# Performance work log

Hardware: AMD Instinct MI355X
Metric: run time of the kernel (lower is better)

## Reference

```python
import jax, jax.numpy as jnp
import numpy as np

N, D_IN, D_OUT, N_CTRS, K = 16384, 64, 64, 512, 16


def setup_inputs() -> dict:
    key = jax.random.key(0)
    k1, k2, k3, k4 = jax.random.split(key, 4)
    x = jax.random.normal(k1, (N, D_IN), dtype=jnp.float32)
    ctrs = jax.random.normal(k2, (N_CTRS, D_IN), dtype=jnp.float32)
    Wv = jax.random.normal(k3, (N_CTRS, D_IN, D_OUT), dtype=jnp.float32) * 0.02
    Ov = jax.random.normal(k4, (N_CTRS, D_OUT), dtype=jnp.float32) * 0.02
    return {"x": x, "ctrs": ctrs, "Wv": Wv, "Ov": Ov, "k": K}


def reference(x, ctrs, Wv, Ov, k):
    n = x.shape[0]
    # squared distances via expansion (same math as sum((x-c)^2), avoids [n,C,d] blowup)
    x2 = jnp.sum(x * x, axis=1, keepdims=True)            # [n,1]
    c2 = jnp.sum(ctrs * ctrs, axis=1)                     # [C]
    dist_sq = x2 + c2[None, :] - 2.0 * (x @ ctrs.T)       # [n,C]
    # k nearest centers; softmax over negative squared distances of the k selected
    neg_top, idx = jax.lax.top_k(-dist_sq, k)             # [n,k] each
    scores = jax.nn.softmax(neg_top, axis=1)              # [n,k]
    # dense soft-assignment matrix (only k nonzeros per row), as in the torch code
    A = jnp.zeros_like(dist_sq).at[jnp.arange(n)[:, None], idx].set(scores)  # [n,C]
    # per-token affine mix: sum_c A[n,c] * (x[n] @ Wv[c] + Ov[c])
    scored_weights = jnp.einsum('nc,cgp->ngp', A, Wv)     # [n,d_in,d_out]
    out = jnp.einsum('ngp,ng->np', scored_weights, x) + A @ Ov  # [n,d_out]
    return out
```

## Files before the change

### kernel.cpp

```cpp
#include <hip/hip_runtime.h>
#include <hip/hip_fp16.h>

#define N_TOK 16384
#define D 64
#define NC 512
#define KSEL 16
#define NPAIR (N_TOK * KSEL)
#define PADCAP 327168

typedef __attribute__((ext_vector_type(8))) short short8;
typedef __attribute__((ext_vector_type(8))) unsigned short ushort8;
typedef __attribute__((ext_vector_type(16))) float float16;

__device__ __forceinline__ unsigned fkey(float f) {
    unsigned u = __float_as_uint(f);
    return (u & 0x80000000u) ? ~u : (u | 0x80000000u);
}
__device__ __forceinline__ float funkey(unsigned k) {
    unsigned u = (k & 0x80000000u) ? (k & 0x7fffffffu) : ~k;
    return __uint_as_float(u);
}
__device__ __forceinline__ unsigned short bfr(float f) {
    unsigned u = __float_as_uint(f);
    return (unsigned short)((u + 0x7FFFu + ((u >> 16) & 1u)) >> 16);
}
__device__ __forceinline__ float b2f(unsigned short h) {
    return __uint_as_float((unsigned)h << 16);
}
__device__ __forceinline__ unsigned pk2(unsigned short a, unsigned short b) {
    return (unsigned)a | ((unsigned)b << 16);
}

__device__ __forceinline__ void ins16(unsigned (&run)[16], unsigned k) {
    #pragma unroll
    for (int r = 0; r < 16; ++r) {
        unsigned mx = run[r] > k ? run[r] : k;
        unsigned mn = run[r] > k ? k : run[r];
        run[r] = mx; k = mn;
    }
}

__global__ __launch_bounds__(256, 4) void topk14_kernel(
    const float* __restrict__ x, const float* __restrict__ ctrs,
    unsigned* __restrict__ pk) {
    __shared__ __align__(16) unsigned char pool[35328];
    unsigned short* Cbf = (unsigned short*)pool;
    unsigned* Sbk = (unsigned*)pool;
    unsigned* mbp = (unsigned*)pool;
    float* c2s = (float*)(pool + 34816);

    const int t = threadIdx.x;
    const int lane = t & 63;
    const int wv = t >> 6;
    const int mrow = lane & 31;
    const int half = lane >> 5;
    const int tb = blockIdx.x >> 2;
    const int p = blockIdx.x & 3;
    const int base = tb * 64;
    const int cbase = p * 128;
    const int trow = (wv & 1) * 32;
    const int cgrp = (wv >> 1) * 64;

    {
        const int r = t >> 1, q = t & 1;
        const float4* cp = (const float4*)(ctrs + (cbase + r) * D + q * 32);
        unsigned short* Ch = Cbf + r * 136 + q * 32;
        float s2 = 0.f;
        #pragma unroll
        for (int i = 0; i < 8; ++i) {
            float4 v = cp[i];
            s2 += v.x * v.x + v.y * v.y + v.z * v.z + v.w * v.w;
            unsigned short h0 = bfr(v.x), h1 = bfr(v.y), h2 = bfr(v.z), h3 = bfr(v.w);
            unsigned short l0 = bfr(v.x - b2f(h0)), l1 = bfr(v.y - b2f(h1));
            unsigned short l2 = bfr(v.z - b2f(h2)), l3 = bfr(v.w - b2f(h3));
            *(uint2*)(Ch + 4 * i)      = make_uint2(pk2(h0, h1), pk2(h2, h3));
            *(uint2*)(Ch + 64 + 4 * i) = make_uint2(pk2(l0, l1), pk2(l2, l3));
        }
        s2 += __shfl_xor(s2, 1);
        c2s[r] = s2;
    }

    short8 ah[4], al[4];
    {
        const float* xp = x + (base + trow + mrow) * D + half * 8;
        #pragma unroll
        for (int kt = 0; kt < 4; ++kt) {
            float4 u = *(const float4*)(xp + kt * 16);
            float4 v = *(const float4*)(xp + kt * 16 + 4);
            float c[8] = {u.x, u.y, u.z, u.w, v.x, v.y, v.z, v.w};
            #pragma unroll
            for (int j = 0; j < 8; ++j) {
                unsigned short h = bfr(c[j]);
                ah[kt][j] = (short)h;
                al[kt][j] = (short)bfr(c[j] - b2f(h));
            }
        }
    }
    __syncthreads();

    float16 acc0 = {0.f,0.f,0.f,0.f,0.f,0.f,0.f,0.f,0.f,0.f,0.f,0.f,0.f,0.f,0.f,0.f};
    float16 acc1 = acc0;

    const unsigned short* B0 = Cbf + (cgrp + mrow) * 136 + half * 8;
    const unsigned short* B1 = Cbf + (cgrp + 32 + mrow) * 136 + half * 8;
    #pragma unroll
    for (int kt = 0; kt < 4; ++kt) {
        short8 bh0 = *(const short8*)(B0 + kt * 16);
        short8 bh1 = *(const short8*)(B1 + kt * 16);
        short8 bl0 = *(const short8*)(B0 + 64 + kt * 16);
        short8 bl1 = *(const short8*)(B1 + 64 + kt * 16);
        acc0 = __builtin_amdgcn_mfma_f32_32x32x16_bf16(ah[kt], bh0, acc0, 0, 0, 0);
        acc1 = __builtin_amdgcn_mfma_f32_32x32x16_bf16(ah[kt], bh1, acc1, 0, 0, 0);
        acc0 = __builtin_amdgcn_mfma_f32_32x32x16_bf16(al[kt], bh0, acc0, 0, 0, 0);
        acc1 = __builtin_amdgcn_mfma_f32_32x32x16_bf16(al[kt], bh1, acc1, 0, 0, 0);
        acc0 = __builtin_amdgcn_mfma_f32_32x32x16_bf16(ah[kt], bl0, acc0, 0, 0, 0);
        acc1 = __builtin_amdgcn_mfma_f32_32x32x16_bf16(ah[kt], bl1, acc1, 0, 0, 0);
    }
    __syncthreads();

    {
        float ca = c2s[cgrp + mrow];
        float cb = c2s[cgrp + 32 + mrow];
        #pragma unroll
        for (int reg = 0; reg < 16; ++reg) {
            int tokrow = trow + (reg & 3) + 8 * (reg >> 2) + 4 * half;
            float sa = fmaf(2.f, acc0[reg], -ca);
            float sb = fmaf(2.f, acc1[reg], -cb);
            Sbk[tokrow * 132 + cgrp + mrow] =
                (fkey(sa) & 0xFFFFFE00u) | (unsigned)(cbase + cgrp + mrow);
            Sbk[tokrow * 132 + cgrp + 32 + mrow] =
                (fkey(sb) & 0xFFFFFE00u) | (unsigned)(cbase + cgrp + 32 + mrow);
        }
    }
    __syncthreads();

    const int tok = t & 63;
    const int h = t >> 6;
    unsigned run[16];
    #pragma unroll
    for (int r = 0; r < 16; ++r) run[r] = 0u;
    #pragma unroll
    for (int i = 0; i < 8; ++i) {
        int cq = ((i + tok) & 7) ^ ((tok >> 3) & 7);
        uint4 kv = *(const uint4*)(Sbk + tok * 132 + 32 * h + 4 * cq);
        ins16(run, kv.x); ins16(run, kv.y); ins16(run, kv.z); ins16(run, kv.w);
    }
    __syncthreads();

    {
        uint4* dst = (uint4*)(mbp + tok * 68 + h * 16);
        dst[0] = make_uint4(run[0], run[1], run[2], run[3]);
        dst[1] = make_uint4(run[4], run[5], run[6], run[7]);
        dst[2] = make_uint4(run[8], run[9], run[10], run[11]);
        dst[3] = make_uint4(run[12], run[13], run[14], run[15]);
    }
    __syncthreads();

    if (t < 64) {
        const unsigned* pm = mbp + t * 68;
        unsigned hv[4]; int pos[4];
        #pragma unroll
        for (int w = 0; w < 4; ++w) { pos[w] = 0; hv[w] = pm[w * 16]; }
        unsigned mm[16];
        #pragma unroll
        for (int r = 0; r < 16; ++r) {
            unsigned m = hv[0];
            #pragma unroll
            for (int w = 1; w < 4; ++w) m = m > hv[w] ? m : hv[w];
            mm[r] = m;
            #pragma unroll
            for (int w = 0; w < 4; ++w) {
                if (hv[w] == m) {
                    ++pos[w];
                    hv[w] = (pos[w] < 16) ? pm[w * 16 + pos[w]] : 0u;
                }
            }
        }
        uint4* dst = (uint4*)(pk + (size_t)(base + t) * 64 + p * 16);
        dst[0] = make_uint4(mm[0], mm[1], mm[2], mm[3]);
        dst[1] = make_uint4(mm[4], mm[5], mm[6], mm[7]);
        dst[2] = make_uint4(mm[8], mm[9], mm[10], mm[11]);
        dst[3] = make_uint4(mm[12], mm[13], mm[14], mm[15]);
    }
}

__global__ __launch_bounds__(256) void topmerge_kernel(
    const unsigned* __restrict__ pk, float* __restrict__ scores,
    int* __restrict__ sidx, int* __restrict__ hist) {
    __shared__ int lhist[NC];
    const int t = threadIdx.x;
    lhist[t] = 0; lhist[t + 256] = 0;
    __syncthreads();
    const int n = blockIdx.x * 256 + t;
    const unsigned* p = pk + (size_t)n * 64;
    unsigned h[4]; int pos[4];
    #pragma unroll
    for (int w = 0; w < 4; ++w) { pos[w] = 0; h[w] = p[w * 16]; }
    float vals[16]; int ids[16];
    #pragma unroll
    for (int r = 0; r < KSEL; ++r) {
        unsigned m = h[0];
        #pragma unroll
        for (int w = 1; w < 4; ++w) m = m > h[w] ? m : h[w];
        vals[r] = funkey(m);
        ids[r] = (int)(m & 511u);
        #pragma unroll
        for (int w = 0; w < 4; ++w) {
            if (h[w] == m) {
                ++pos[w];
                h[w] = (pos[w] < KSEL) ? p[w * 16 + pos[w]] : 0u;
            }
        }
    }
    float mx = vals[0];
    float e[16]; float sum = 0.f;
    #pragma unroll
    for (int r = 0; r < KSEL; ++r) { e[r] = __expf(vals[r] - mx); sum += e[r]; }
    float inv = 1.f / sum;
    #pragma unroll
    for (int q = 0; q < 4; ++q) {
        *(float4*)(scores + n * KSEL + 4 * q) =
            make_float4(e[4*q] * inv, e[4*q+1] * inv, e[4*q+2] * inv, e[4*q+3] * inv);
        *(int4*)(sidx + n * KSEL + 4 * q) =
            make_int4(ids[4*q], ids[4*q+1], ids[4*q+2], ids[4*q+3]);
    }
    #pragma unroll
    for (int r = 0; r < KSEL; ++r) atomicAdd(&lhist[ids[r]], 1);
    __syncthreads();
    { int hv = lhist[t]; if (hv) atomicAdd(&hist[t], hv); }
    { int hv = lhist[t + 256]; if (hv) atomicAdd(&hist[t + 256], hv); }
}

__global__ __launch_bounds__(512) void scan2_kernel(const int* __restrict__ hist,
                                                    int* __restrict__ cursor,
                                                    int* __restrict__ meta) {
    __shared__ int buf[2][NC];
    int t = threadIdx.x;
    int pad = (hist[t] + 127) & ~127;
    buf[0][t] = pad;
    __syncthreads();
    int a = 0;
    for (int d = 1; d < NC; d <<= 1) {
        int val = buf[a][t] + (t >= d ? buf[a][t - d] : 0);
        buf[1 - a][t] = val;
        __syncthreads();
        a = 1 - a;
    }
    int incl = buf[a][t];
    cursor[t] = incl - pad;
    if (t == NC - 1) meta[0] = incl;
}

__global__ __launch_bounds__(256) void scatter4_kernel(
    const int* __restrict__ sidx, const float* __restrict__ scores,
    int* __restrict__ cursor, int* __restrict__ tokentab,
    float* __restrict__ scotab) {
    __shared__ int lh[NC];
    __shared__ int lbase[NC];
    const int t = threadIdx.x;
    for (int i = t; i < NC; i += 256) lh[i] = 0;
    __syncthreads();
    const int base_e = blockIdx.x * 1024;
    int myc[4];
    #pragma unroll
    for (int i = 0; i < 4; ++i) {
        int c = sidx[base_e + t + 256 * i];
        myc[i] = c;
        atomicAdd(&lh[c], 1);
    }
    __syncthreads();
    for (int i = t; i < NC; i += 256) {
        int h = lh[i];
        lbase[i] = h ? atomicAdd(&cursor[i], h) : 0;
        lh[i] = 0;
    }
    __syncthreads();
    #pragma unroll
    for (int i = 0; i < 4; ++i) {
        int e = base_e + t + 256 * i;
        int c = myc[i];
        int pos = lbase[c] + atomicAdd(&lh[c], 1);
        tokentab[pos] = (c << 19) | e;
        scotab[pos] = scores[e];
    }
}

__global__ __launch_bounds__(256) void mix16_kernel(
    const float* __restrict__ x, const float* __restrict__ Wv,
    const float* __restrict__ Ov, const int* __restrict__ tokentab,
    const float* __restrict__ scotab, const int* __restrict__ meta,
    __half* __restrict__ partial) {
    __shared__ __align__(16) unsigned short Wt[64 * 72];
    __shared__ int eT[128];
    __shared__ float sT[128];

    const int t = threadIdx.x;
    const int base = blockIdx.x * 128;
    if (base >= meta[0]) return;

    const int c = (int)(((unsigned)tokentab[base]) >> 19);

    {
        const float* Wp = Wv + c * (D * D) + (t & 63);
        const int gb = (t >> 6) * 16;
        #pragma unroll
        for (int g = 0; g < 16; g += 2) {
            float v0 = Wp[(gb + g) * 64];
            float v1 = Wp[(gb + g + 1) * 64];
            unsigned pkw = (unsigned)bfr(v0) | ((unsigned)bfr(v1) << 16);
            *(unsigned*)&Wt[(t & 63) * 72 + gb + g] = pkw;
        }
    }
    if (t < 128) {
        unsigned w = (unsigned)tokentab[base + t];
        eT[t] = (int)(w & 0x7FFFFu);
        sT[t] = scotab[base + t];
    }
    __syncthreads();

    const int lane = t & 63;
    const int wv = t >> 6;
    const int mrow = lane & 31;
    const int half = lane >> 5;
    const int row = wv * 32 + mrow;

    const int   mye = eT[row];
    const int   myn = (mye < NPAIR) ? (mye >> 4) : 0;
    const float mys = sT[row];

    const float* xp = x + myn * D + half * 8;
    float4 f[8];
    #pragma unroll
    for (int kt = 0; kt < 4; ++kt) {
        f[2 * kt]     = *(const float4*)(xp + kt * 16);
        f[2 * kt + 1] = *(const float4*)(xp + kt * 16 + 4);
    }
    short8 a[4];
    #pragma unroll
    for (int kt = 0; kt < 4; ++kt) {
        float4 u = f[2 * kt], v = f[2 * kt + 1];
        a[kt][0] = (short)bfr(u.x * mys); a[kt][1] = (short)bfr(u.y * mys);
        a[kt][2] = (short)bfr(u.z * mys); a[kt][3] = (short)bfr(u.w * mys);
        a[kt][4] = (short)bfr(v.x * mys); a[kt][5] = (short)bfr(v.y * mys);
        a[kt][6] = (short)bfr(v.z * mys); a[kt][7] = (short)bfr(v.w * mys);
    }

    float16 acc0 = {0.f,0.f,0.f,0.f,0.f,0.f,0.f,0.f,0.f,0.f,0.f,0.f,0.f,0.f,0.f,0.f};
    float16 acc1 = {0.f,0.f,0.f,0.f,0.f,0.f,0.f,0.f,0.f,0.f,0.f,0.f,0.f,0.f,0.f,0.f};

    const unsigned short* B0 = Wt + mrow * 72;
    const unsigned short* B1 = Wt + (mrow + 32) * 72;
    #pragma unroll
    for (int kt = 0; kt < 4; ++kt) {
        short8 b0 = *(const short8*)(B0 + kt * 16 + half * 8);
        short8 b1 = *(const short8*)(B1 + kt * 16 + half * 8);
        acc0 = __builtin_amdgcn_mfma_f32_32x32x16_bf16(a[kt], b0, acc0, 0, 0, 0);
        acc1 = __builtin_amdgcn_mfma_f32_32x32x16_bf16(a[kt], b1, acc1, 0, 0, 0);
    }

    const float ov0 = Ov[c * D + mrow];
    const float ov1 = Ov[c * D + 32 + mrow];
    #pragma unroll
    for (int reg = 0; reg < 16; ++reg) {
        int orow = wv * 32 + (reg & 3) + 8 * (reg >> 2) + 4 * half;
        float s = sT[orow];
        int e = eT[orow];
        if (e < NPAIR) {
            __half* dst = partial + (size_t)e * D;
            dst[mrow]      = __float2half(acc0[reg] + s * ov0);
            dst[32 + mrow] = __float2half(acc1[reg] + s * ov1);
        }
    }
}

__global__ __launch_bounds__(256) void redu2_kernel(
    const __half* __restrict__ partial, float* __restrict__ out) {
    const int g = blockIdx.x * 256 + threadIdx.x;
    const int n = g >> 3;
    const int d8 = (g & 7) * 8;
    const __half* p = partial + (size_t)n * (KSEL * D) + d8;
    float s[8] = {0.f, 0.f, 0.f, 0.f, 0.f, 0.f, 0.f, 0.f};
    #pragma unroll
    for (int r = 0; r < KSEL; ++r) {
        ushort8 v = *(const ushort8*)(p + r * D);
        #pragma unroll
        for (int j = 0; j < 8; ++j)
            s[j] += __half2float(__ushort_as_half((unsigned short)v[j]));
    }
    float* o = out + n * D + d8;
    *(float4*)(o)     = make_float4(s[0], s[1], s[2], s[3]);
    *(float4*)(o + 4) = make_float4(s[4], s[5], s[6], s[7]);
}

__global__ __launch_bounds__(256) void mix14_kernel(
    const float* __restrict__ x, const float* __restrict__ Wv,
    const float* __restrict__ Ov, const int* __restrict__ tokentab,
    const float* __restrict__ scotab, const int* __restrict__ meta,
    float* __restrict__ out) {
    __shared__ __align__(16) unsigned short Wt[64 * 72];
    __shared__ int tT[128];
    __shared__ float sT[128];

    const int t = threadIdx.x;
    const int base = blockIdx.x * 128;
    if (base >= meta[0]) return;

    const int c = (int)(((unsigned)tokentab[base]) >> 19);

    {
        const float* Wp = Wv + c * (D * D) + (t & 63);
        const int gb = (t >> 6) * 16;
        #pragma unroll
        for (int g = 0; g < 16; g += 2) {
            float v0 = Wp[(gb + g) * 64];
            float v1 = Wp[(gb + g + 1) * 64];
            unsigned pkw = (unsigned)bfr(v0) | ((unsigned)bfr(v1) << 16);
            *(unsigned*)&Wt[(t & 63) * 72 + gb + g] = pkw;
        }
    }
    if (t < 128) {
        unsigned w = (unsigned)tokentab[base + t];
        tT[t] = (int)((w & 0x7FFFFu) >> 4);
        sT[t] = scotab[base + t];
    }
    __syncthreads();

    const int lane = t & 63;
    const int wv = t >> 6;
    const int mrow = lane & 31;
    const int half = lane >> 5;
    const int row = wv * 32 + mrow;

    const int   myn = tT[row];
    const float mys = sT[row];

    const float* xp = x + myn * D + half * 8;
    float4 f[8];
    #pragma unroll
    for (int kt = 0; kt < 4; ++kt) {
        f[2 * kt]     = *(const float4*)(xp + kt * 16);
        f[2 * kt + 1] = *(const float4*)(xp + kt * 16 + 4);
    }
    short8 a[4];
    #pragma unroll
    for (int kt = 0; kt < 4; ++kt) {
        float4 u = f[2 * kt], v = f[2 * kt + 1];
        a[kt][0] = (short)bfr(u.x * mys); a[kt][1] = (short)bfr(u.y * mys);
        a[kt][2] = (short)bfr(u.z * mys); a[kt][3] = (short)bfr(u.w * mys);
        a[kt][4] = (short)bfr(v.x * mys); a[kt][5] = (short)bfr(v.y * mys);
        a[kt][6] = (short)bfr(v.z * mys); a[kt][7] = (short)bfr(v.w * mys);
    }

    float16 acc0 = {0.f,0.f,0.f,0.f,0.f,0.f,0.f,0.f,0.f,0.f,0.f,0.f,0.f,0.f,0.f,0.f};
    float16 acc1 = {0.f,0.f,0.f,0.f,0.f,0.f,0.f,0.f,0.f,0.f,0.f,0.f,0.f,0.f,0.f,0.f};

    const unsigned short* B0 = Wt + mrow * 72;
    const unsigned short* B1 = Wt + (mrow + 32) * 72;
    #pragma unroll
    for (int kt = 0; kt < 4; ++kt) {
        short8 b0 = *(const short8*)(B0 + kt * 16 + half * 8);
        short8 b1 = *(const short8*)(B1 + kt * 16 + half * 8);
        acc0 = __builtin_amdgcn_mfma_f32_32x32x16_bf16(a[kt], b0, acc0, 0, 0, 0);
        acc1 = __builtin_amdgcn_mfma_f32_32x32x16_bf16(a[kt], b1, acc1, 0, 0, 0);
    }

    const float ov0 = Ov[c * D + mrow];
    const float ov1 = Ov[c * D + 32 + mrow];
    #pragma unroll
    for (int reg = 0; reg < 16; ++reg) {
        int orow = wv * 32 + (reg & 3) + 8 * (reg >> 2) + 4 * half;
        float s = sT[orow];
        if (s != 0.f) {
            int n = tT[orow];
            unsafeAtomicAdd(out + n * D + mrow,      acc0[reg] + s * ov0);
            unsafeAtomicAdd(out + n * D + 32 + mrow, acc1[reg] + s * ov1);
        }
    }
}

extern "C" void kernel_launch(void* const* d_in, const int* in_sizes, int n_in,
                              void* d_out, int out_size, void* d_ws, size_t ws_size,
                              hipStream_t stream) {
    const float* x    = (const float*)d_in[0];
    const float* ctrs = (const float*)d_in[1];
    const float* Wv   = (const float*)d_in[2];
    const float* Ov   = (const float*)d_in[3];
    float* out = (float*)d_out;

    int*   hist     = (int*)d_ws + 512;
    int*   meta     = (int*)d_ws + 1024;
    int*   cursor   = (int*)d_ws + 2048;
    float* scores   = (float*)d_ws + 2560;
    int*   sidx     = (int*)d_ws + 2560 + NPAIR;
    int*   tokentab = (int*)d_ws + 2560 + 2 * NPAIR;
    float* scotab   = (float*)d_ws + 2560 + 2 * NPAIR + PADCAP;
    __half* partial = (__half*)((int*)d_ws + 2560 + 2 * NPAIR + 2 * PADCAP);
    unsigned* pkbuf = (unsigned*)partial;

    const size_t need = ((size_t)2560 + 2 * (size_t)NPAIR + 2 * (size_t)PADCAP) * 4
                      + (size_t)NPAIR * D * 2;
    const bool fast = ws_size >= need;

    hipMemsetAsync(hist, 0, NC * sizeof(int), stream);
    if (fast) {
        hipMemsetAsync(tokentab, 0xFF, (size_t)PADCAP * sizeof(int), stream);
    } else {
        hipMemsetAsync(out, 0, (size_t)N_TOK * D * sizeof(float), stream);
        hipMemsetAsync(scotab, 0, (size_t)PADCAP * sizeof(float), stream);
        hipMemsetAsync(tokentab, 0, (size_t)PADCAP * sizeof(int), stream);
    }
    hipLaunchKernelGGL(topk14_kernel, dim3((N_TOK / 64) * 4), dim3(256), 0, stream,
                       x, ctrs, pkbuf);
    hipLaunchKernelGGL(topmerge_kernel, dim3(N_TOK / 256), dim3(256), 0, stream,
                       pkbuf, scores, sidx, hist);
    hipLaunchKernelGGL(scan2_kernel, dim3(1), dim3(512), 0, stream, hist, cursor, meta);
    hipLaunchKernelGGL(scatter4_kernel, dim3(256), dim3(256), 0, stream,
                       sidx, scores, cursor, tokentab, scotab);
    if (fast) {
        hipLaunchKernelGGL(mix16_kernel, dim3(PADCAP / 128), dim3(256), 0, stream,
                           x, Wv, Ov, tokentab, scotab, meta, partial);
        hipLaunchKernelGGL(redu2_kernel, dim3(N_TOK * 8 / 256), dim3(256), 0, stream,
                           partial, out);
    } else {
        hipLaunchKernelGGL(mix14_kernel, dim3(PADCAP / 128), dim3(256), 0, stream,
                           x, Wv, Ov, tokentab, scotab, meta, out);
    }
}
```

Before: 144.5 us.

## Precompute bf16 splits in prep kernel and fuse scan into scatter

After: 143.3 us. About the same (-0.8%).

```diff
diff --git a/kernel.cpp b/kernel.cpp
--- a/kernel.cpp
+++ b/kernel.cpp
@@ -27,9 +27,6 @@
 __device__ __forceinline__ float b2f(unsigned short h) {
     return __uint_as_float((unsigned)h << 16);
 }
-__device__ __forceinline__ unsigned pk2(unsigned short a, unsigned short b) {
-    return (unsigned)a | ((unsigned)b << 16);
-}
 
 __device__ __forceinline__ void ins16(unsigned (&run)[16], unsigned k) {
     #pragma unroll
@@ -40,8 +37,53 @@
     }
 }
 
-__global__ __launch_bounds__(256, 4) void topk14_kernel(
+__global__ __launch_bounds__(256) void prep_kernel(
     const float* __restrict__ x, const float* __restrict__ ctrs,
+    unsigned short* __restrict__ xh, unsigned short* __restrict__ xl,
+    unsigned short* __restrict__ cbf, float* __restrict__ c2g) {
+    const int b = blockIdx.x, t = threadIdx.x;
+    if (b < 512) {
+        int g = b * 256 + t;
+        int row = g >> 3, seg = g & 7;
+        const float4* xp = (const float4*)(x + row * 64 + seg * 8);
+        float4 u = xp[0], v = xp[1];
+        float c[8] = {u.x, u.y, u.z, u.w, v.x, v.y, v.z, v.w};
+        ushort8 h, l;
+        #pragma unroll
+        for (int j = 0; j < 8; ++j) {
+            h[j] = bfr(c[j]);
+            l[j] = bfr(c[j] - b2f(h[j]));
+        }
+        *(ushort8*)(xh + row * 64 + seg * 8) = h;
+        *(ushort8*)(xl + row * 64 + seg * 8) = l;
+    } else {
+        int g = (b - 512) * 256 + t;
+        int c = g >> 1, q = g & 1;
+        const float4* cp = (const float4*)(ctrs + c * D + q * 32);
+        unsigned short* Ch = cbf + c * 136 + q * 32;
+        float s2 = 0.f;
+        #pragma unroll
+        for (int i = 0; i < 8; ++i) {
+            float4 v = cp[i];
+            s2 += v.x * v.x + v.y * v.y + v.z * v.z + v.w * v.w;
+            unsigned short h0 = bfr(v.x), h1 = bfr(v.y), h2 = bfr(v.z), h3 = bfr(v.w);
+            unsigned short l0 = bfr(v.x - b2f(h0)), l1 = bfr(v.y - b2f(h1));
+            unsigned short l2 = bfr(v.z - b2f(h2)), l3 = bfr(v.w - b2f(h3));
+            *(uint2*)(Ch + 4 * i) =
+                make_uint2((unsigned)h0 | ((unsigned)h1 << 16),
+                           (unsigned)h2 | ((unsigned)h3 << 16));
+            *(uint2*)(Ch + 64 + 4 * i) =
+                make_uint2((unsigned)l0 | ((unsigned)l1 << 16),
+                           (unsigned)l2 | ((unsigned)l3 << 16));
+        }
+        s2 += __shfl_xor(s2, 1);
+        c2g[c] = s2;
+    }
+}
+
+__global__ __launch_bounds__(256, 4) void topk15_kernel(
+    const unsigned short* __restrict__ xh, const unsigned short* __restrict__ xl,
+    const unsigned short* __restrict__ cbf, const float* __restrict__ c2g,
     unsigned* __restrict__ pk) {
     __shared__ __align__(16) unsigned char pool[35328];
     unsigned short* Cbf = (unsigned short*)pool;
@@ -62,38 +104,25 @@
     const int cgrp = (wv >> 1) * 64;
 
     {
-        const int r = t >> 1, q = t & 1;
-        const float4* cp = (const float4*)(ctrs + (cbase + r) * D + q * 32);
-        unsigned short* Ch = Cbf + r * 136 + q * 32;
-        float s2 = 0.f;
-        #pragma unroll
-        for (int i = 0; i < 8; ++i) {
-            float4 v = cp[i];
-            s2 += v.x * v.x + v.y * v.y + v.z * v.z + v.w * v.w;
-            unsigned short h0 = bfr(v.x), h1 = bfr(v.y), h2 = bfr(v.z), h3 = bfr(v.w);
-            unsigned short l0 = bfr(v.x - b2f(h0)), l1 = bfr(v.y - b2f(h1));
-            unsigned short l2 = bfr(v.z - b2f(h2)), l3 = bfr(v.w - b2f(h3));
-            *(uint2*)(Ch + 4 * i)      = make_uint2(pk2(h0, h1), pk2(h2, h3));
-            *(uint2*)(Ch + 64 + 4 * i) = make_uint2(pk2(l0, l1), pk2(l2, l3));
-        }
-        s2 += __shfl_xor(s2, 1);
-        c2s[r] = s2;
+        const uint4* src = (const uint4*)(cbf + (size_t)cbase * 136);
+        uint4* dst = (uint4*)pool;
+        #pragma unroll
+        for (int i = 0; i < 8; ++i) dst[t + 256 * i] = src[t + 256 * i];
+        if (t < 128) {
+            dst[2048 + t] = src[2048 + t];
+            c2s[t] = c2g[cbase + t];
+        }
     }
 
     short8 ah[4], al[4];
     {
-        const float* xp = x + (base + trow + mrow) * D + half * 8;
+        const int xrow = base + trow + mrow;
+        const unsigned short* xph = xh + (size_t)xrow * 64 + half * 8;
+        const unsigned short* xpl = xl + (size_t)xrow * 64 + half * 8;
         #pragma unroll
         for (int kt = 0; kt < 4; ++kt) {
-            float4 u = *(const float4*)(xp + kt * 16);
-            float4 v = *(const float4*)(xp + kt * 16 + 4);
-            float c[8] = {u.x, u.y, u.z, u.w, v.x, v.y, v.z, v.w};
-            #pragma unroll
-            for (int j = 0; j < 8; ++j) {
-                unsigned short h = bfr(c[j]);
-                ah[kt][j] = (short)h;
-                al[kt][j] = (short)bfr(c[j] - b2f(h));
-            }
+            ah[kt] = *(const short8*)(xph + kt * 16);
+            al[kt] = *(const short8*)(xpl + kt * 16);
         }
     }
     __syncthreads();
@@ -231,35 +260,35 @@
     { int hv = lhist[t + 256]; if (hv) atomicAdd(&hist[t + 256], hv); }
 }
 
-__global__ __launch_bounds__(512) void scan2_kernel(const int* __restrict__ hist,
-                                                    int* __restrict__ cursor,
-                                                    int* __restrict__ meta) {
+__global__ __launch_bounds__(256) void scatter5_kernel(
+    const int* __restrict__ hist, const int* __restrict__ sidx,
+    const float* __restrict__ scores, int* __restrict__ cursor,
+    int* __restrict__ tokentab, float* __restrict__ scotab,
+    int* __restrict__ meta) {
     __shared__ int buf[2][NC];
-    int t = threadIdx.x;
-    int pad = (hist[t] + 127) & ~127;
-    buf[0][t] = pad;
-    __syncthreads();
-    int a = 0;
-    for (int d = 1; d < NC; d <<= 1) {
-        int val = buf[a][t] + (t >= d ? buf[a][t - d] : 0);
-        buf[1 - a][t] = val;
-        __syncthreads();
-        a = 1 - a;
-    }
-    int incl = buf[a][t];
-    cursor[t] = incl - pad;
-    if (t == NC - 1) meta[0] = incl;
-}
-
-__global__ __launch_bounds__(256) void scatter4_kernel(
-    const int* __restrict__ sidx, const float* __restrict__ scores,
-    int* __restrict__ cursor, int* __restrict__ tokentab,
-    float* __restrict__ scotab) {
+    __shared__ int sb[NC];
     __shared__ int lh[NC];
     __shared__ int lbase[NC];
     const int t = threadIdx.x;
-    for (int i = t; i < NC; i += 256) lh[i] = 0;
-    __syncthreads();
+
+    int h0 = hist[t], h1 = hist[t + 256];
+    int p0 = (h0 + 127) & ~127, p1 = (h1 + 127) & ~127;
+    buf[0][t] = p0; buf[0][t + 256] = p1;
+    __syncthreads();
+    int a = 0;
+    for (int d = 1; d < NC; d <<= 1) {
+        int v0 = buf[a][t] + (t >= d ? buf[a][t - d] : 0);
+        int v1 = buf[a][t + 256] + (t + 256 >= d ? buf[a][t + 256 - d] : 0);
+        buf[1 - a][t] = v0; buf[1 - a][t + 256] = v1;
+        __syncthreads();
+        a ^= 1;
+    }
+    sb[t] = buf[a][t] - p0;
+    sb[t + 256] = buf[a][t + 256] - p1;
+    if (t == 255) meta[0] = buf[a][NC - 1];
+    lh[t] = 0; lh[t + 256] = 0;
+    __syncthreads();
+
     const int base_e = blockIdx.x * 1024;
     int myc[4];
     #pragma unroll
@@ -271,7 +300,7 @@
     __syncthreads();
     for (int i = t; i < NC; i += 256) {
         int h = lh[i];
-        lbase[i] = h ? atomicAdd(&cursor[i], h) : 0;
+        lbase[i] = h ? (sb[i] + atomicAdd(&cursor[i], h)) : 0;
         lh[i] = 0;
     }
     __syncthreads();
@@ -487,21 +516,44 @@
     const float* Ov   = (const float*)d_in[3];
     float* out = (float*)d_out;
 
-    int*   hist     = (int*)d_ws + 512;
-    int*   meta     = (int*)d_ws + 1024;
-    int*   cursor   = (int*)d_ws + 2048;
-    float* scores   = (float*)d_ws + 2560;
-    int*   sidx     = (int*)d_ws + 2560 + NPAIR;
-    int*   tokentab = (int*)d_ws + 2560 + 2 * NPAIR;
-    float* scotab   = (float*)d_ws + 2560 + 2 * NPAIR + PADCAP;
-    __half* partial = (__half*)((int*)d_ws + 2560 + 2 * NPAIR + 2 * PADCAP);
-    unsigned* pkbuf = (unsigned*)partial;
-
-    const size_t need = ((size_t)2560 + 2 * (size_t)NPAIR + 2 * (size_t)PADCAP) * 4
-                      + (size_t)NPAIR * D * 2;
+    const size_t OFF_META = 0;
+    const size_t OFF_HIST = 512;
+    const size_t OFF_CUR  = 1024;
+    const size_t OFF_SCO  = 2560;
+    const size_t OFF_SIDX = OFF_SCO + NPAIR;
+    const size_t OFF_TTAB = OFF_SIDX + NPAIR;
+    const size_t OFF_STAB = OFF_TTAB + PADCAP;
+    const size_t OFF_PK   = OFF_STAB + PADCAP;
+    const size_t OFF_XH   = OFF_PK + (size_t)N_TOK * 16;
+    const size_t PK_INTS  = (size_t)N_TOK * 64;
+    const size_t XH_INTS  = (size_t)N_TOK * 32;
+    const size_t CBF_INTS = (size_t)NC * 68;
+    const size_t O_PK   = OFF_STAB + PADCAP;
+    const size_t O_XH   = O_PK + PK_INTS;
+    const size_t O_XL   = O_XH + XH_INTS;
+    const size_t O_CBF  = O_XL + XH_INTS;
+    const size_t O_C2   = O_CBF + CBF_INTS;
+    const size_t O_PART = O_C2 + 512;
+    const size_t PART_INTS = (size_t)NPAIR * 32;
+
+    int*    meta     = (int*)d_ws + OFF_META;
+    int*    hist     = (int*)d_ws + OFF_HIST;
+    int*    cursor   = (int*)d_ws + OFF_CUR;
+    float*  scores   = (float*)d_ws + OFF_SCO;
+    int*    sidx     = (int*)d_ws + OFF_SIDX;
+    int*    tokentab = (int*)d_ws + OFF_TTAB;
+    float*  scotab   = (float*)d_ws + OFF_STAB;
+    unsigned* pkbuf  = (unsigned*)((int*)d_ws + O_PK);
+    unsigned short* xh  = (unsigned short*)((int*)d_ws + O_XH);
+    unsigned short* xl  = (unsigned short*)((int*)d_ws + O_XL);
+    unsigned short* cbf = (unsigned short*)((int*)d_ws + O_CBF);
+    float*  c2g      = (float*)((int*)d_ws + O_C2);
+    __half* partial  = (__half*)((int*)d_ws + O_PART);
+
+    const size_t need = (O_PART + PART_INTS) * 4;
     const bool fast = ws_size >= need;
 
-    hipMemsetAsync(hist, 0, NC * sizeof(int), stream);
+    hipMemsetAsync(hist, 0, 2 * NC * sizeof(int), stream);
     if (fast) {
         hipMemsetAsync(tokentab, 0xFF, (size_t)PADCAP * sizeof(int), stream);
     } else {
@@ -509,13 +561,14 @@
         hipMemsetAsync(scotab, 0, (size_t)PADCAP * sizeof(float), stream);
         hipMemsetAsync(tokentab, 0, (size_t)PADCAP * sizeof(int), stream);
     }
-    hipLaunchKernelGGL(topk14_kernel, dim3((N_TOK / 64) * 4), dim3(256), 0, stream,
-                       x, ctrs, pkbuf);
+    hipLaunchKernelGGL(prep_kernel, dim3(516), dim3(256), 0, stream,
+                       x, ctrs, xh, xl, cbf, c2g);
+    hipLaunchKernelGGL(topk15_kernel, dim3((N_TOK / 64) * 4), dim3(256), 0, stream,
+                       xh, xl, cbf, c2g, pkbuf);
     hipLaunchKernelGGL(topmerge_kernel, dim3(N_TOK / 256), dim3(256), 0, stream,
                        pkbuf, scores, sidx, hist);
-    hipLaunchKernelGGL(scan2_kernel, dim3(1), dim3(512), 0, stream, hist, cursor, meta);
-    hipLaunchKernelGGL(scatter4_kernel, dim3(256), dim3(256), 0, stream,
-                       sidx, scores, cursor, tokentab, scotab);
+    hipLaunchKernelGGL(scatter5_kernel, dim3(256), dim3(256), 0, stream,
+                       hist, sidx, scores, cursor, tokentab, scotab, meta);
     if (fast) {
         hipLaunchKernelGGL(mix16_kernel, dim3(PADCAP / 128), dim3(256), 0, stream,
                            x, Wv, Ov, tokentab, scotab, meta, partial);
```
